# Kernel optimization log

Measured on AMD Instinct MI355X. Metric: run time of the kernel, lower is better.

The kernel has to match this reference:

```python
import jax, jax.numpy as jnp
import numpy as np

EMBED_DIM = 1024
NUM_HEADS = 16
HEAD_DIM = EMBED_DIM // NUM_HEADS
LAMBDA_ENTANGLE = 0.35


def setup_inputs() -> dict:
    key = jax.random.key(0)
    ks = jax.random.split(key, 10)
    B, S, D = 2, 2048, EMBED_DIM
    init = 1.0 / np.sqrt(D)  # mimic nn.Linear uniform init scale
    x = jax.random.normal(ks[0], (B, S, D), dtype=jnp.float32)
    Wq = jax.random.uniform(ks[1], (D, D), jnp.float32, -init, init)
    bq = jax.random.uniform(ks[2], (D,), jnp.float32, -init, init)
    Wk = jax.random.uniform(ks[3], (D, D), jnp.float32, -init, init)
    bk = jax.random.uniform(ks[4], (D,), jnp.float32, -init, init)
    Wv = jax.random.uniform(ks[5], (D, D), jnp.float32, -init, init)
    bv = jax.random.uniform(ks[6], (D,), jnp.float32, -init, init)
    Wo = jax.random.uniform(ks[7], (D, D), jnp.float32, -init, init)
    bo = jax.random.uniform(ks[8], (D,), jnp.float32, -init, init)
    J_attn = jax.random.normal(ks[9], (NUM_HEADS, HEAD_DIM, HEAD_DIM), dtype=jnp.float32) * 0.02
    lambda_attn = jnp.asarray(LAMBDA_ENTANGLE, dtype=jnp.float32)
    return {"x": x, "Wq": Wq, "bq": bq, "Wk": Wk, "bk": bk, "Wv": Wv, "bv": bv,
            "Wo": Wo, "bo": bo, "J_attn": J_attn, "lambda_attn": lambda_attn}


def reference(x, Wq, bq, Wk, bk, Wv, bv, Wo, bo, J_attn, lambda_attn):
    B, S, D = x.shape
    H, Hd = NUM_HEADS, HEAD_DIM
    scale = jnp.sqrt(jnp.asarray(Hd, dtype=x.dtype))

    def heads(W, b):
        # (B,S,D) @ (D,D) + b -> (B,H,S,Hd)
        y = jnp.einsum('bsd,ed->bse', x, W) + b
        return y.reshape(B, S, H, Hd).transpose(0, 2, 1, 3)

    Q = heads(Wq, bq)
    K = heads(Wk, bk)
    V = heads(Wv, bv)

    scores = jnp.einsum('bhid,bhjd->bhij', Q, K) / scale
    # bilinear entanglement correction: tanh(Q) J tanh(K)^T
    QJ = jnp.einsum('bhid,hde->bhie', jnp.tanh(Q), J_attn)  # (B,H,S,Hd)
    delta = jnp.einsum('bhie,bhje->bhij', QJ, jnp.tanh(K))
    scores = scores + lambda_attn * delta

    causal = jnp.triu(jnp.ones((S, S), dtype=bool), k=1)
    scores = jnp.where(causal, -jnp.inf, scores)

    probs = jax.nn.softmax(scores, axis=-1)
    out = jnp.einsum('bhij,bhjd->bhid', probs, V)  # (B,H,S,Hd)
    out = out.transpose(0, 2, 1, 3).reshape(B, S, D)
    return jnp.einsum('bsd,ed->bse', out, Wo) + bo
```

## Files before the change

kernel.cpp:

```cpp
#include <hip/hip_runtime.h>
#include <hip/hip_bf16.h>

typedef unsigned short u16;
typedef __bf16 bf16x8 __attribute__((ext_vector_type(8)));
typedef float f32x4 __attribute__((ext_vector_type(4)));
typedef unsigned short u16x4 __attribute__((ext_vector_type(4)));

#define MFMA16(a, b, c) __builtin_amdgcn_mfma_f32_16x16x32_bf16(a, b, c, 0, 0, 0)

#define EMB 1024
#define SEQ 2048
#define NH 16
#define HD 64
#define LOG2E 1.4426950408889634f

#define GLOAD_LDS16(g, l) __builtin_amdgcn_global_load_lds( \
    (const __attribute__((address_space(1))) unsigned int*)(g), \
    (__attribute__((address_space(3))) unsigned int*)(l), 16, 0, 0)

__device__ __forceinline__ float b2f(u16 u) {
    union { unsigned int i; float f; } v; v.i = ((unsigned int)u) << 16; return v.f;
}
__device__ __forceinline__ u16 f2b(float f) {
    __hip_bfloat16 h = __float2bfloat16(f);
    return *reinterpret_cast<u16*>(&h);
}
__device__ __forceinline__ u16x4 pack4(float a, float b, float c, float d) {
    union { __hip_bfloat162 h2[2]; u16x4 u; } r;
    r.h2[0] = __float22bfloat162_rn(float2{a, b});
    r.h2[1] = __float22bfloat162_rn(float2{c, d});
    return r.u;
}
__device__ __forceinline__ bf16x8 ldfrag(const u16* p) {
    return *reinterpret_cast<const bf16x8*>(p);
}
__device__ __forceinline__ bf16x8 cvt8(const float* p) {
    const float4 a = *reinterpret_cast<const float4*>(p);
    const float4 b = *reinterpret_cast<const float4*>(p + 4);
    union { u16x4 q[2]; bf16x8 v; } r;
    r.q[0] = pack4(a.x, a.y, a.z, a.w);
    r.q[1] = pack4(b.x, b.y, b.z, b.w);
    return r.v;
}
__device__ __forceinline__ float fast_tanh(float x) {
    float t = exp2f(x * (2.0f * LOG2E));
    return 1.0f - 2.0f * __builtin_amdgcn_rcpf(t + 1.0f);
}
__device__ __forceinline__ bf16x8 tanh8(bf16x8 v) {
    union { bf16x8 v; u16 u[8]; } in; in.v = v;
    float o[8];
#pragma unroll
    for (int e = 0; e < 8; e++) o[e] = fast_tanh(b2f(in.u[e]));
    union { u16x4 q[2]; bf16x8 v; } r;
    r.q[0] = pack4(o[0], o[1], o[2], o[3]);
    r.q[1] = pack4(o[4], o[5], o[6], o[7]);
    return r.v;
}

__global__ __launch_bounds__(256) void cvt_all(
        const float* __restrict__ x,  const float* __restrict__ Wq,
        const float* __restrict__ Wk, const float* __restrict__ Wv,
        const float* __restrict__ Wo, u16* __restrict__ dst)
{
    size_t i = ((size_t)blockIdx.x * 256 + threadIdx.x) * 8;
    const float* src; size_t off;
    if (i < 4194304) { src = x; off = i; }
    else {
        size_t j = i - 4194304; int w = (int)(j >> 20); off = j & 1048575;
        src = (w == 0) ? Wq : (w == 1) ? Wk : (w == 2) ? Wv : Wo;
    }
    *(bf16x8*)&dst[i] = cvt8(src + off);
}

template<int MI>
__global__ __launch_bounds__(256, 4) void gemm_epi(
        const u16* __restrict__ A,
        const u16* __restrict__ W0, const float* __restrict__ B0,
        const u16* __restrict__ W1, const float* __restrict__ B1,
        const u16* __restrict__ W2, const float* __restrict__ B2,
        const float* __restrict__ lam,
        u16* __restrict__ Qa, u16* __restrict__ Ka, u16* __restrict__ Vt,
        float* __restrict__ out, int modeBase)
{
    const int mode = modeBase + blockIdx.z;
    const u16* W; const float* bias;
    if (blockIdx.z == 0)      { W = W0; bias = B0; }
    else if (blockIdx.z == 1) { W = W1; bias = B1; }
    else                      { W = W2; bias = B2; }

    __shared__ __attribute__((aligned(16))) u16 sA[MI * 32 * 64];
    __shared__ __attribute__((aligned(16))) u16 sB[128 * 64];

    const int t = threadIdx.x;
    const int w = t >> 6, L = t & 63;
    const int wm = w >> 1, wn = w & 1;
    const int lr = L & 15, lq = L >> 4;
    const int wbase = t & 192;
    const int m0 = blockIdx.y * (MI * 32), n0 = blockIdx.x * 128;

    f32x4 acc[MI][4];
#pragma unroll
    for (int i = 0; i < MI; i++)
#pragma unroll
        for (int j = 0; j < 4; j++) { f32x4 z = {0.f, 0.f, 0.f, 0.f}; acc[i][j] = z; }

    for (int k0 = 0; k0 < EMB; k0 += 64) {
        __syncthreads();
#pragma unroll
        for (int q = 0; q < MI; q++) {
            int c = q * 256 + t;
            int row = c >> 3, cc = c & 7;
            int col8 = cc ^ (row & 7);
            GLOAD_LDS16(&A[(size_t)(m0 + row) * EMB + k0 + col8 * 8],
                        &sA[(q * 256 + wbase) * 8]);
        }
#pragma unroll
        for (int q = 0; q < 4; q++) {
            int c = q * 256 + t;
            int row = c >> 3, cc = c & 7;
            int col8 = cc ^ (row & 7);
            GLOAD_LDS16(&W[(size_t)(n0 + row) * EMB + k0 + col8 * 8],
                        &sB[(q * 256 + wbase) * 8]);
        }
        __syncthreads();
#pragma unroll
        for (int s = 0; s < 2; s++) {
            bf16x8 af[MI], bfr[4];
#pragma unroll
            for (int mi = 0; mi < MI; mi++) {
                int row = wm * (MI * 16) + mi * 16 + lr;
                af[mi] = ldfrag(&sA[(row * 8 + ((s * 4 + lq) ^ (row & 7))) * 8]);
            }
#pragma unroll
            for (int ni = 0; ni < 4; ni++) {
                int row = wn * 64 + ni * 16 + lr;
                bfr[ni] = ldfrag(&sB[(row * 8 + ((s * 4 + lq) ^ (row & 7))) * 8]);
            }
#pragma unroll
            for (int mi = 0; mi < MI; mi++)
#pragma unroll
                for (int ni = 0; ni < 4; ni++)
                    acc[mi][ni] = MFMA16(af[mi], bfr[ni], acc[mi][ni]);
        }
    }

    const float lamf = lam[0];
#pragma unroll
    for (int mi = 0; mi < MI; mi++)
#pragma unroll
        for (int ni = 0; ni < 4; ni++) {
            int mb = m0 + wm * (MI * 16) + mi * 16 + lq * 4;
            int n  = n0 + wn * 64 + ni * 16 + lr;
            float bv = bias[n];
            if (mode == 3) {
#pragma unroll
                for (int r = 0; r < 4; r++)
                    out[(size_t)(mb + r) * EMB + n] = acc[mi][ni][r] + bv;
            } else {
                int b = mb >> 11, s0 = mb & 2047;
                int h = n >> 6,  d = n & 63;
                if (mode == 0) {
#pragma unroll
                    for (int r = 0; r < 4; r++) {
                        float val = acc[mi][ni][r] + bv;
                        size_t i128 = ((size_t)(b * NH + h) * SEQ + s0 + r) * 128 + d;
                        Qa[i128]      = f2b(val * (0.125f * LOG2E));
                        Qa[i128 + 64] = f2b(lamf * LOG2E * fast_tanh(val));
                    }
                } else if (mode == 1) {
#pragma unroll
                    for (int r = 0; r < 4; r++) {
                        float val = acc[mi][ni][r] + bv;
                        Ka[((size_t)(b * NH + h) * SEQ + s0 + r) * 128 + d] = f2b(val);
                    }
                } else {
                    u16x4 pk = pack4(acc[mi][ni][0] + bv, acc[mi][ni][1] + bv,
                                     acc[mi][ni][2] + bv, acc[mi][ni][3] + bv);
                    *(u16x4*)&Vt[((size_t)(b * NH + h) * HD + d) * SEQ + s0] = pk;
                }
            }
        }
}

__global__ __launch_bounds__(256) void ukern(
        const float* __restrict__ J, u16* __restrict__ Ka)
{
    __shared__ __attribute__((aligned(16))) u16 sJ[64 * 72];
    const int t = threadIdx.x, w = t >> 6, L = t & 63, lr = L & 15, lq = L >> 4;
    const int rt = blockIdx.x, bh = blockIdx.y, h = bh & 15;

#pragma unroll
    for (int i = 0; i < 2; i++) {
        int c = t + 256 * i;
        int row = c >> 3, col = (c & 7) * 8;
        *(bf16x8*)&sJ[row * 72 + col] = cvt8(&J[(size_t)h * 4096 + row * 64 + col]);
    }
    __syncthreads();

    const u16* krow = &Ka[((size_t)bh * SEQ + rt * 64 + w * 16 + lr) * 128];
    bf16x8 a0 = tanh8(ldfrag(krow + lq * 8));
    bf16x8 a1 = tanh8(ldfrag(krow + lq * 8 + 32));
#pragma unroll
    for (int nt = 0; nt < 4; nt++) {
        f32x4 acc = {0.f, 0.f, 0.f, 0.f};
        acc = MFMA16(a0, ldfrag(&sJ[(nt * 16 + lr) * 72 + lq * 8]), acc);
        acc = MFMA16(a1, ldfrag(&sJ[(nt * 16 + lr) * 72 + lq * 8 + 32]), acc);
#pragma unroll
        for (int r = 0; r < 4; r++) {
            int j = rt * 64 + w * 16 + lq * 4 + r;
            Ka[((size_t)bh * SEQ + j) * 128 + 64 + nt * 16 + lr] = f2b(acc[r]);
        }
    }
}

__global__ __launch_bounds__(256) void flash(
        const u16* __restrict__ Qa, const u16* __restrict__ Ka,
        const u16* __restrict__ Vt, u16* __restrict__ attn)
{
    __shared__ __attribute__((aligned(16))) u16 sK[64 * 128];
    __shared__ __attribute__((aligned(16))) u16 sVt[64 * 64];
    __shared__ __attribute__((aligned(16))) u16 sP[128 * 72];

    const int t = threadIdx.x, w = t >> 6, L = t & 63, lr = L & 15, lq = L >> 4;
    const int bh = blockIdx.x & 31, p = blockIdx.x >> 5;
    const int qt = blockIdx.y ? 15 - p : p;
    const int qm = qt * 128;
    const int i_l = w * 16 + lr;
    const int wbase = t & 192;
    const u16* Kbase = Ka + (size_t)bh * SEQ * 128;
    const u16* Vbase = Vt + (size_t)bh * HD * SEQ;

    bf16x8 qf[2][4];
#pragma unroll
    for (int g = 0; g < 2; g++) {
        const u16* qrow = Qa + ((size_t)bh * SEQ + qm + g * 64 + i_l) * 128;
#pragma unroll
        for (int s = 0; s < 4; s++) qf[g][s] = ldfrag(qrow + s * 32 + lq * 8);
    }

    f32x4 Ot[2][4];
#pragma unroll
    for (int g = 0; g < 2; g++)
#pragma unroll
        for (int i = 0; i < 4; i++) { f32x4 z = {0.f, 0.f, 0.f, 0.f}; Ot[g][i] = z; }
    float lsum[2] = {0.f, 0.f};

    const int ktmax = 2 * qt + 1;
    for (int kt = 0; kt <= ktmax; kt++) {
        const int kn = kt * 64;
        __syncthreads();
#pragma unroll
        for (int q = 0; q < 4; q++) {
            int cch = q * 256 + t;
            int row = cch >> 4, cc = cch & 15;
            int col8 = cc ^ (row & 15);
            GLOAD_LDS16(&Kbase[(size_t)(kn + row) * 128 + col8 * 8],
                        &sK[(q * 256 + wbase) * 8]);
        }
#pragma unroll
        for (int q = 0; q < 2; q++) {
            int cch = q * 256 + t;
            int d = cch >> 3, cc = cch & 7;
            int j8 = cc ^ (d & 7);
            GLOAD_LDS16(&Vbase[(size_t)d * SEQ + kn + j8 * 8],
                        &sVt[(q * 256 + wbase) * 8]);
        }
        __syncthreads();

        f32x4 sc[2][4];
#pragma unroll
        for (int g = 0; g < 2; g++)
#pragma unroll
            for (int mt = 0; mt < 4; mt++) { f32x4 z = {0.f,0.f,0.f,0.f}; sc[g][mt] = z; }
#pragma unroll
        for (int mt = 0; mt < 4; mt++) {
            int j = mt * 16 + lr;
#pragma unroll
            for (int s = 0; s < 4; s++) {
                bf16x8 kf = ldfrag(&sK[(j * 16 + ((s * 4 + lq) ^ (j & 15))) * 8]);
                sc[0][mt] = MFMA16(kf, qf[0][s], sc[0][mt]);
                sc[1][mt] = MFMA16(kf, qf[1][s], sc[1][mt]);
            }
        }
        if (kt >= ktmax - 1) {
            const int thr0 = (kt == ktmax) ? -1  : i_l;
            const int thr1 = (kt == ktmax) ? i_l : 63;
#pragma unroll
            for (int mt = 0; mt < 4; mt++)
#pragma unroll
                for (int r = 0; r < 4; r++) {
                    int j = mt * 16 + lq * 4 + r;
                    if (j > thr0) sc[0][mt][r] = -INFINITY;
                    if (j > thr1) sc[1][mt][r] = -INFINITY;
                }
        }
#pragma unroll
        for (int g = 0; g < 2; g++) {
#pragma unroll
            for (int mt = 0; mt < 4; mt++)
#pragma unroll
                for (int r = 0; r < 4; r++) {
                    float e = exp2f(sc[g][mt][r]);
                    sc[g][mt][r] = e;
                    lsum[g] += e;
                }
#pragma unroll
            for (int mt = 0; mt < 4; mt++)
                *(u16x4*)&sP[(g * 64 + i_l) * 72 + mt * 16 + lq * 4] =
                    pack4(sc[g][mt][0], sc[g][mt][1], sc[g][mt][2], sc[g][mt][3]);
        }
#pragma unroll
        for (int s2 = 0; s2 < 2; s2++) {
            bf16x8 pf0 = ldfrag(&sP[(i_l) * 72 + s2 * 32 + lq * 8]);
            bf16x8 pf1 = ldfrag(&sP[(64 + i_l) * 72 + s2 * 32 + lq * 8]);
#pragma unroll
            for (int mt = 0; mt < 4; mt++) {
                int d = mt * 16 + lr;
                bf16x8 vf = ldfrag(&sVt[(d * 8 + ((s2 * 4 + lq) ^ (d & 7))) * 8]);
                Ot[0][mt] = MFMA16(vf, pf0, Ot[0][mt]);
                Ot[1][mt] = MFMA16(vf, pf1, Ot[1][mt]);
            }
        }
    }

    const int b = bh >> 4, h = bh & 15;
#pragma unroll
    for (int g = 0; g < 2; g++) {
        float ls = lsum[g];
        ls += __shfl_xor(ls, 16);
        ls += __shfl_xor(ls, 32);
        const float r0 = __builtin_amdgcn_rcpf(ls);
        const float inv = r0 * (2.0f - ls * r0);
        const size_t base = ((size_t)(b * SEQ + qm + g * 64 + i_l)) * EMB + h * HD;
#pragma unroll
        for (int mt = 0; mt < 4; mt++)
            *(u16x4*)&attn[base + mt * 16 + lq * 4] =
                pack4(Ot[g][mt][0] * inv, Ot[g][mt][1] * inv,
                      Ot[g][mt][2] * inv, Ot[g][mt][3] * inv);
    }
}

extern "C" void kernel_launch(void* const* d_in, const int* in_sizes, int n_in,
                              void* d_out, int out_size, void* d_ws, size_t ws_size,
                              hipStream_t stream)
{
    const float* x   = (const float*)d_in[0];
    const float* Wq  = (const float*)d_in[1];
    const float* bq  = (const float*)d_in[2];
    const float* Wk  = (const float*)d_in[3];
    const float* bk  = (const float*)d_in[4];
    const float* Wv  = (const float*)d_in[5];
    const float* bv  = (const float*)d_in[6];
    const float* Wo  = (const float*)d_in[7];
    const float* bo  = (const float*)d_in[8];
    const float* J   = (const float*)d_in[9];
    const float* lam = (const float*)d_in[10];

    u16* ws  = (u16*)d_ws;
    u16* xb  = ws;
    u16* Wqb = xb  + (size_t)4096 * 1024;
    u16* Wkb = Wqb + (size_t)1024 * 1024;
    u16* Wvb = Wkb + (size_t)1024 * 1024;
    u16* Wob = Wvb + (size_t)1024 * 1024;
    u16* Qa  = Wob + (size_t)1024 * 1024;
    u16* Ka  = Qa  + (size_t)32 * 2048 * 128;
    u16* Vt  = Ka  + (size_t)32 * 2048 * 128;
    u16* attn = xb;
    float* dout = (float*)d_out;

    dim3 blk(256);
    cvt_all<<<dim3(4096), blk, 0, stream>>>(x, Wq, Wk, Wv, Wo, ws);
    gemm_epi<4><<<dim3(8, 32, 3), blk, 0, stream>>>(
        xb, Wqb, bq, Wkb, bk, Wvb, bv, lam, Qa, Ka, Vt, dout, 0);
    ukern<<<dim3(32, 32), blk, 0, stream>>>(J, Ka);
    flash<<<dim3(256, 2), blk, 0, stream>>>(Qa, Ka, Vt, attn);
    gemm_epi<2><<<dim3(8, 64, 1), blk, 0, stream>>>(
        attn, Wob, bo, Wob, bo, Wob, bo, lam, Qa, Ka, Vt, dout, 3);
}
```

Measured before the change: 210.8 us.

## Swap MFMA operands for vectorized GEMM epilogues and drop flash LDS staging

The GEMM kernel gains a template flag that swaps the MFMA operand order, so each lane holds four consecutive output columns. This allows float4 bias loads and vectorized u16x4/float4 stores for Q, K and the output projection. The V projection keeps the old layout in a separate launch for its transposed store. The flash kernel no longer stages K and V tiles through LDS with barriers and instead loads MFMA fragments straight from global memory. That removes LDS traffic and syncs per tile, but each wave now re-reads K/V from cache, and the GEMM is split into two launches.

```diff
diff --git a/kernel.cpp b/kernel.cpp
--- a/kernel.cpp
+++ b/kernel.cpp
@@ -72,21 +72,19 @@
     *(bf16x8*)&dst[i] = cvt8(src + off);
 }
 
-template<int MI>
+template<int MI, int SW>
 __global__ __launch_bounds__(256, 4) void gemm_epi(
         const u16* __restrict__ A,
         const u16* __restrict__ W0, const float* __restrict__ B0,
         const u16* __restrict__ W1, const float* __restrict__ B1,
-        const u16* __restrict__ W2, const float* __restrict__ B2,
         const float* __restrict__ lam,
         u16* __restrict__ Qa, u16* __restrict__ Ka, u16* __restrict__ Vt,
         float* __restrict__ out, int modeBase)
 {
     const int mode = modeBase + blockIdx.z;
     const u16* W; const float* bias;
-    if (blockIdx.z == 0)      { W = W0; bias = B0; }
-    else if (blockIdx.z == 1) { W = W1; bias = B1; }
-    else                      { W = W2; bias = B2; }
+    if (blockIdx.z == 0) { W = W0; bias = B0; }
+    else                 { W = W1; bias = B1; }
 
     __shared__ __attribute__((aligned(16))) u16 sA[MI * 32 * 64];
     __shared__ __attribute__((aligned(16))) u16 sB[128 * 64];
@@ -139,47 +137,56 @@
 #pragma unroll
             for (int mi = 0; mi < MI; mi++)
 #pragma unroll
-                for (int ni = 0; ni < 4; ni++)
-                    acc[mi][ni] = MFMA16(af[mi], bfr[ni], acc[mi][ni]);
+                for (int ni = 0; ni < 4; ni++) {
+                    if constexpr (SW) acc[mi][ni] = MFMA16(bfr[ni], af[mi], acc[mi][ni]);
+                    else              acc[mi][ni] = MFMA16(af[mi], bfr[ni], acc[mi][ni]);
+                }
         }
     }
 
     const float lamf = lam[0];
-#pragma unroll
-    for (int mi = 0; mi < MI; mi++)
-#pragma unroll
-        for (int ni = 0; ni < 4; ni++) {
-            int mb = m0 + wm * (MI * 16) + mi * 16 + lq * 4;
-            int n  = n0 + wn * 64 + ni * 16 + lr;
-            float bv = bias[n];
-            if (mode == 3) {
-#pragma unroll
-                for (int r = 0; r < 4; r++)
-                    out[(size_t)(mb + r) * EMB + n] = acc[mi][ni][r] + bv;
-            } else {
+    if constexpr (SW) {
+#pragma unroll
+        for (int mi = 0; mi < MI; mi++)
+#pragma unroll
+            for (int ni = 0; ni < 4; ni++) {
+                int m  = m0 + wm * (MI * 16) + mi * 16 + lr;
+                int nb = n0 + wn * 64 + ni * 16 + lq * 4;
+                float4 bv4 = *(const float4*)&bias[nb];
+                float v0 = acc[mi][ni][0] + bv4.x, v1 = acc[mi][ni][1] + bv4.y;
+                float v2 = acc[mi][ni][2] + bv4.z, v3 = acc[mi][ni][3] + bv4.w;
+                if (mode == 3) {
+                    *(float4*)&out[(size_t)m * EMB + nb] = float4{v0, v1, v2, v3};
+                } else {
+                    int b = m >> 11, s0 = m & 2047;
+                    int h = nb >> 6, d = nb & 63;
+                    size_t i128 = ((size_t)(b * NH + h) * SEQ + s0) * 128 + d;
+                    if (mode == 0) {
+                        const float cs = 0.125f * LOG2E, ct = lamf * LOG2E;
+                        *(u16x4*)&Qa[i128] = pack4(v0 * cs, v1 * cs, v2 * cs, v3 * cs);
+                        *(u16x4*)&Qa[i128 + 64] =
+                            pack4(ct * fast_tanh(v0), ct * fast_tanh(v1),
+                                  ct * fast_tanh(v2), ct * fast_tanh(v3));
+                    } else {
+                        *(u16x4*)&Ka[i128] = pack4(v0, v1, v2, v3);
+                    }
+                }
+            }
+    } else {
+#pragma unroll
+        for (int mi = 0; mi < MI; mi++)
+#pragma unroll
+            for (int ni = 0; ni < 4; ni++) {
+                int mb = m0 + wm * (MI * 16) + mi * 16 + lq * 4;
+                int n  = n0 + wn * 64 + ni * 16 + lr;
+                float bv = bias[n];
                 int b = mb >> 11, s0 = mb & 2047;
                 int h = n >> 6,  d = n & 63;
-                if (mode == 0) {
-#pragma unroll
-                    for (int r = 0; r < 4; r++) {
-                        float val = acc[mi][ni][r] + bv;
-                        size_t i128 = ((size_t)(b * NH + h) * SEQ + s0 + r) * 128 + d;
-                        Qa[i128]      = f2b(val * (0.125f * LOG2E));
-                        Qa[i128 + 64] = f2b(lamf * LOG2E * fast_tanh(val));
-                    }
-                } else if (mode == 1) {
-#pragma unroll
-                    for (int r = 0; r < 4; r++) {
-                        float val = acc[mi][ni][r] + bv;
-                        Ka[((size_t)(b * NH + h) * SEQ + s0 + r) * 128 + d] = f2b(val);
-                    }
-                } else {
-                    u16x4 pk = pack4(acc[mi][ni][0] + bv, acc[mi][ni][1] + bv,
-                                     acc[mi][ni][2] + bv, acc[mi][ni][3] + bv);
-                    *(u16x4*)&Vt[((size_t)(b * NH + h) * HD + d) * SEQ + s0] = pk;
-                }
-            }
-        }
+                u16x4 pk = pack4(acc[mi][ni][0] + bv, acc[mi][ni][1] + bv,
+                                 acc[mi][ni][2] + bv, acc[mi][ni][3] + bv);
+                *(u16x4*)&Vt[((size_t)(b * NH + h) * HD + d) * SEQ + s0] = pk;
+            }
+    }
 }
 
 __global__ __launch_bounds__(256) void ukern(
@@ -217,8 +224,6 @@
         const u16* __restrict__ Qa, const u16* __restrict__ Ka,
         const u16* __restrict__ Vt, u16* __restrict__ attn)
 {
-    __shared__ __attribute__((aligned(16))) u16 sK[64 * 128];
-    __shared__ __attribute__((aligned(16))) u16 sVt[64 * 64];
     __shared__ __attribute__((aligned(16))) u16 sP[128 * 72];
 
     const int t = threadIdx.x, w = t >> 6, L = t & 63, lr = L & 15, lq = L >> 4;
@@ -226,7 +231,6 @@
     const int qt = blockIdx.y ? 15 - p : p;
     const int qm = qt * 128;
     const int i_l = w * 16 + lr;
-    const int wbase = t & 192;
     const u16* Kbase = Ka + (size_t)bh * SEQ * 128;
     const u16* Vbase = Vt + (size_t)bh * HD * SEQ;
 
@@ -248,36 +252,16 @@
     const int ktmax = 2 * qt + 1;
     for (int kt = 0; kt <= ktmax; kt++) {
         const int kn = kt * 64;
-        __syncthreads();
-#pragma unroll
-        for (int q = 0; q < 4; q++) {
-            int cch = q * 256 + t;
-            int row = cch >> 4, cc = cch & 15;
-            int col8 = cc ^ (row & 15);
-            GLOAD_LDS16(&Kbase[(size_t)(kn + row) * 128 + col8 * 8],
-                        &sK[(q * 256 + wbase) * 8]);
-        }
-#pragma unroll
-        for (int q = 0; q < 2; q++) {
-            int cch = q * 256 + t;
-            int d = cch >> 3, cc = cch & 7;
-            int j8 = cc ^ (d & 7);
-            GLOAD_LDS16(&Vbase[(size_t)d * SEQ + kn + j8 * 8],
-                        &sVt[(q * 256 + wbase) * 8]);
-        }
-        __syncthreads();
 
         f32x4 sc[2][4];
 #pragma unroll
-        for (int g = 0; g < 2; g++)
-#pragma unroll
-            for (int mt = 0; mt < 4; mt++) { f32x4 z = {0.f,0.f,0.f,0.f}; sc[g][mt] = z; }
+        for (int mt = 0; mt < 4; mt++) { f32x4 z = {0.f,0.f,0.f,0.f}; sc[0][mt] = z; sc[1][mt] = z; }
 #pragma unroll
         for (int mt = 0; mt < 4; mt++) {
-            int j = mt * 16 + lr;
+            const u16* krow = Kbase + (size_t)(kn + mt * 16 + lr) * 128 + lq * 8;
 #pragma unroll
             for (int s = 0; s < 4; s++) {
-                bf16x8 kf = ldfrag(&sK[(j * 16 + ((s * 4 + lq) ^ (j & 15))) * 8]);
+                bf16x8 kf = ldfrag(krow + s * 32);
                 sc[0][mt] = MFMA16(kf, qf[0][s], sc[0][mt]);
                 sc[1][mt] = MFMA16(kf, qf[1][s], sc[1][mt]);
             }
@@ -315,8 +299,8 @@
             bf16x8 pf1 = ldfrag(&sP[(64 + i_l) * 72 + s2 * 32 + lq * 8]);
 #pragma unroll
             for (int mt = 0; mt < 4; mt++) {
-                int d = mt * 16 + lr;
-                bf16x8 vf = ldfrag(&sVt[(d * 8 + ((s2 * 4 + lq) ^ (d & 7))) * 8]);
+                bf16x8 vf = ldfrag(Vbase + (size_t)(mt * 16 + lr) * SEQ
+                                   + kn + s2 * 32 + lq * 8);
                 Ot[0][mt] = MFMA16(vf, pf0, Ot[0][mt]);
                 Ot[1][mt] = MFMA16(vf, pf1, Ot[1][mt]);
             }
@@ -370,10 +354,12 @@
 
     dim3 blk(256);
     cvt_all<<<dim3(4096), blk, 0, stream>>>(x, Wq, Wk, Wv, Wo, ws);
-    gemm_epi<4><<<dim3(8, 32, 3), blk, 0, stream>>>(
-        xb, Wqb, bq, Wkb, bk, Wvb, bv, lam, Qa, Ka, Vt, dout, 0);
+    gemm_epi<4, 1><<<dim3(8, 32, 2), blk, 0, stream>>>(
+        xb, Wqb, bq, Wkb, bk, lam, Qa, Ka, Vt, dout, 0);
+    gemm_epi<4, 0><<<dim3(8, 32, 1), blk, 0, stream>>>(
+        xb, Wvb, bv, Wvb, bv, lam, Qa, Ka, Vt, dout, 2);
     ukern<<<dim3(32, 32), blk, 0, stream>>>(J, Ka);
     flash<<<dim3(256, 2), blk, 0, stream>>>(Qa, Ka, Vt, attn);
-    gemm_epi<2><<<dim3(8, 64, 1), blk, 0, stream>>>(
-        attn, Wob, bo, Wob, bo, Wob, bo, lam, Qa, Ka, Vt, dout, 3);
-}
+    gemm_epi<2, 1><<<dim3(8, 64, 1), blk, 0, stream>>>(
+        attn, Wob, bo, Wob, bo, lam, Qa, Ka, Vt, dout, 3);
+}
```

Result: slower. 298.5 us (+41.6%).
